# Kernel tuning notes

Measured on AMD Instinct MI355X. Metric: run time of the kernel, lower is better.

## Reference

```python
import math
import numpy as np
import jax, jax.numpy as jnp

LMAX1, LMAX2, LMAX3 = 20, 10, 5
B_IN, RES1, RES2, RES3 = 60, 20, 10, 6
BATCH = 8


def _fact(n):
    return math.factorial(n)


def wigner_d(l, betas):
    # small Wigner-d, complex-m ordering m=-l..l; betas: [N] -> [N, 2l+1, 2l+1]
    betas = np.asarray(betas, dtype=np.float64)
    cb, sb = np.cos(betas / 2.0), np.sin(betas / 2.0)
    d = np.zeros(betas.shape + (2 * l + 1, 2 * l + 1))
    for i, mp in enumerate(range(-l, l + 1)):
        for j, m in enumerate(range(-l, l + 1)):
            pref = math.sqrt(_fact(l + mp) * _fact(l - mp) * _fact(l + m) * _fact(l - m))
            val = np.zeros_like(betas)
            for k in range(max(0, m - mp), min(l + m, l - mp) + 1):
                den = _fact(l + m - k) * _fact(k) * _fact(mp - m + k) * _fact(l - mp - k)
                val = val + ((-1.0) ** (mp - m + k)) * (pref / den) * cb ** (2 * l + m - mp - 2 * k) * sb ** (mp - m + 2 * k)
            d[..., i, j] = val
    return d


def real_U(l):
    # complex SH -> real SH change of basis
    U = np.zeros((2 * l + 1, 2 * l + 1), dtype=np.complex128)
    U[l, l] = 1.0
    for m in range(1, l + 1):
        s = (-1.0) ** m
        U[l + m, l - m] = 1.0 / math.sqrt(2.0)
        U[l + m, l + m] = s / math.sqrt(2.0)
        U[l - m, l - m] = 1j / math.sqrt(2.0)
        U[l - m, l + m] = -1j * s / math.sqrt(2.0)
    return U


def wigner_d_real(l, betas):
    U = real_U(l)
    d = wigner_d(l, betas).astype(np.complex128)
    return np.einsum('ai,nij,bj->nab', U, d, U.conj()).real


def _trig(ang, l):
    m = np.arange(-l, l + 1)
    return np.cos(np.outer(ang, m)), np.sin(np.outer(ang, m))


def flat_wigner_points(lmax, a, b, g):
    # real Wigner D on arbitrary points via D = Z(alpha) d_real(beta) Z(gamma)
    blocks = []
    for l in range(lmax + 1):
        dr = wigner_d_real(l, b)  # [N,M,M]
        cA, sA = _trig(a, l)
        cG, sG = _trig(g, l)
        T = cG[:, None, :] * dr - sG[:, None, :] * dr[:, :, ::-1]
        D = cA[:, :, None] * T + sA[:, :, None] * T[:, ::-1, :]
        blocks.append(math.sqrt(2 * l + 1) * D.reshape(len(a), -1))
    return np.concatenate(blocks, -1).astype(np.float32)


def flat_wigner_grid(lmax, alphas, betas, gammas):
    # product-grid version, flatten order (alpha, beta, gamma)
    na, nb, ng = len(alphas), len(betas), len(gammas)
    blocks = []
    for l in range(lmax + 1):
        dr = wigner_d_real(l, betas)  # [nb,M,M]
        cA, sA = _trig(alphas, l)
        cG, sG = _trig(gammas, l)
        T = cG[None, :, None, :] * dr[:, None] - sG[None, :, None, :] * dr[:, None, :, ::-1]  # [nb,ng,M,M]
        D = cA[:, None, None, :, None] * T[None] + sA[:, None, None, :, None] * T[None, :, :, ::-1, :]
        blocks.append(math.sqrt(2 * l + 1) * D.reshape(na * nb * ng, -1))
    return np.concatenate(blocks, -1).astype(np.float32)


def sph_points(lmax, a, b):
    # component-normalized real SH: Y_l(alpha,beta) = sqrt(2l+1) D^l(alpha,beta,0)[:,m=0]
    cols = []
    for l in range(lmax + 1):
        dr = wigner_d_real(l, b)[:, :, l]
        cA, sA = _trig(a, l)
        cols.append(math.sqrt(2 * l + 1) * (cA * dr + sA * dr[:, ::-1]))
    return np.concatenate(cols, -1).astype(np.float32)


def sph_grid_cols(lmax, alphas, betas):
    cols = []
    for l in range(lmax + 1):
        dr = wigner_d_real(l, betas)[:, :, l]  # [nb,M]
        cA, sA = _trig(alphas, l)
        Y = cA[None] * dr[:, None] + sA[None] * dr[:, None, ::-1]  # [nb,na,M]
        cols.append(math.sqrt(2 * l + 1) * Y)
    return np.concatenate(cols, -1)


def so3_grid(n):
    a = np.arange(n) / n * 2 * math.pi
    b = (np.arange(n) + 0.5) / n * math.pi
    g = np.arange(n) / n * 2 * math.pi
    return a, b, g


def so3_transforms(lmax_in, lmax_out, n):
    a, b, g = so3_grid(n)
    D_in = flat_wigner_grid(lmax_in, a, b, g)
    D_out = flat_wigner_grid(lmax_out, a, b, g)
    qw = np.tile(np.sin(b)[None, :, None], (n, 1, n)).ravel() * math.pi / (2.0 * n ** 3)
    return jnp.asarray(D_in), jnp.asarray((qw[:, None] * D_out).astype(np.float32))


def s2_near_identity_grid(max_beta=math.pi / 8, n_alpha=8, n_beta=3):
    beta = np.arange(1, n_beta + 1) * max_beta / n_beta
    alpha = np.linspace(0, 2 * math.pi, n_alpha + 1)[:-1]
    A, B = np.meshgrid(alpha, beta, indexing='ij')
    return A.ravel(), B.ravel()


def so3_near_identity_grid(max_beta=math.pi / 8, max_gamma=2 * math.pi, n_alpha=8, n_beta=3, n_gamma=8):
    beta = np.arange(1, n_beta + 1) * max_beta / n_beta
    alpha = np.linspace(0, 2 * math.pi, n_alpha)[:-1]
    pre_gamma = np.linspace(-max_gamma, max_gamma, n_gamma)
    A, B, preC = np.meshgrid(alpha, beta, pre_gamma, indexing='ij')
    return A.ravel(), B.ravel(), (preC - A).ravel()


# ---- constant buffers (built once with numpy, like e3nn register_buffer) ----
_betas = (np.arange(B_IN) + 0.5) / B_IN * math.pi
_alphas = np.arange(B_IN) / B_IN * 2 * math.pi
_Y = sph_grid_cols(LMAX1, _alphas, _betas)  # [nb,na,441]
_qw = np.sin(_betas) * math.pi / (2.0 * B_IN * B_IN)
FROM_S2 = jnp.asarray((_Y * _qw[:, None, None]).reshape(B_IN * B_IN, -1).astype(np.float32))  # [3600,441]

_a2, _b2 = s2_near_identity_grid()
Y_K = jnp.asarray(sph_points(LMAX1, _a2, _b2))  # [24,441]
_a3, _b3, _g3 = so3_near_identity_grid()
D_K2 = jnp.asarray(flat_wigner_points(LMAX2, _a3, _b3, _g3))  # [168,1771]
D_K3 = jnp.asarray(flat_wigner_points(LMAX3, _a3, _b3, _g3))  # [168,286]

D1_IN, D1_BWD = so3_transforms(LMAX1, LMAX2, RES1)  # [8000,12341], [8000,1771]
D2_IN, D2_BWD = so3_transforms(LMAX2, LMAX3, RES2)  # [1000,1771],  [1000,286]
D3_IN, D3_BWD = so3_transforms(LMAX3, 0, RES3)      # [216,286],    [216,1]


def _s2_linear(x, psi, lmax):
    # x [B,f_in,(lmax+1)^2] (mult-1 per l) -> so3 irreps [B,f_out,sum(2l+1)^2]
    B, fi = x.shape[0], x.shape[1]
    outs = []
    for l in range(lmax + 1):
        s, e = l * l, (l + 1) * (l + 1)
        ol = jnp.einsum('bim,iou->boum', x[:, :, s:e], psi[:, :, s:e]) / math.sqrt(fi)
        outs.append(ol.reshape(B, ol.shape[1], -1))
    return jnp.concatenate(outs, axis=-1)


def _so3_linear(x, psi, lmax):
    # block per-l linear: mult (2l+1) -> mult (2l+1)
    B, fi = x.shape[0], x.shape[1]
    outs, off = [], 0
    for l in range(lmax + 1):
        d = 2 * l + 1
        xl = x[:, :, off:off + d * d].reshape(B, fi, d, d)
        pl = psi[:, :, off:off + d * d].reshape(fi, -1, d, d)
        ol = jnp.einsum('bium,iouv->bovm', xl, pl) / math.sqrt(fi * d)
        outs.append(ol.reshape(B, ol.shape[1], -1))
        off += d * d
    return jnp.concatenate(outs, axis=-1)


def _so3_act(x, D_in, D_bwd):
    # SO3Activation: to SO(3) grid, relu, back to (lower) band-limited coeffs
    f = jax.nn.relu(jnp.einsum('bfi,ni->bfn', x, D_in))
    return jnp.einsum('bfn,ni->bfi', f, D_bwd)


def _forward(x, conv1_w, conv2_w, conv3_w, fc_w1, fc_b1, fc_w2, fc_b2):
    B = x.shape[0]
    xg = jnp.swapaxes(x, -1, -2).reshape(B, -1)  # (beta, alpha) grid, flattened
    coeff = (xg @ FROM_S2)[:, None, :]           # FromS2Grid -> [B,1,441]
    psi1 = jnp.einsum('ni,xyn->xyi', Y_K, conv1_w) / math.sqrt(Y_K.shape[0])
    h = _s2_linear(coeff, psi1, LMAX1)           # [B,64,12341]
    h = _so3_act(h, D1_IN, D1_BWD)               # [B,64,1771]
    psi2 = jnp.einsum('ni,xyn->xyi', D_K2, conv2_w) / math.sqrt(D_K2.shape[0])
    h = _so3_linear(h, psi2, LMAX2)              # [B,128,1771]
    h = _so3_act(h, D2_IN, D2_BWD)               # [B,128,286]
    psi3 = jnp.einsum('ni,xyn->xyi', D_K3, conv3_w) / math.sqrt(D_K3.shape[0])
    h = _so3_linear(h, psi3, LMAX3)              # [B,256,286]
    h = _so3_act(h, D3_IN, D3_BWD)[:, :, 0]      # lmax_out=0 -> [B,256]
    h = jax.nn.relu(h @ fc_w1 + fc_b1)           # dropout is identity in eval
    return h @ fc_w2 + fc_b2


def setup_inputs() -> dict:
    key = jax.random.key(0)
    ks = jax.random.split(key, 6)
    return {
        'x': jax.random.normal(ks[0], (BATCH, B_IN, B_IN), dtype=jnp.float32),
        'conv1_w': jax.random.normal(ks[1], (1, 64, 24), dtype=jnp.float32),
        'conv2_w': jax.random.normal(ks[2], (64, 128, 168), dtype=jnp.float32),
        'conv3_w': jax.random.normal(ks[3], (128, 256, 168), dtype=jnp.float32),
        'fc_w1': jax.random.normal(ks[4], (256, 128), dtype=jnp.float32) / math.sqrt(256.0),
        'fc_b1': jnp.zeros((128,), jnp.float32),
        'fc_w2': jax.random.normal(ks[5], (128, 10), dtype=jnp.float32) / math.sqrt(128.0),
        'fc_b2': jnp.zeros((10,), jnp.float32),
    }


def reference(x, conv1_w, conv2_w, conv3_w, fc_w1, fc_b1, fc_w2, fc_b2):
    return _forward(x, conv1_w, conv2_w, conv3_w, fc_w1, fc_b1, fc_w2, fc_b2)
```

## Files before the change

kernel.cpp:

```cpp
#include <hip/hip_runtime.h>

#define PI_D 3.14159265358979323846

constexpr int S_L20 = 12341;
constexpr int S_L10 = 1771;
constexpr int S_L5  = 286;
constexpr int C_L20 = 441;

typedef float f4 __attribute__((ext_vector_type(4)));
typedef float f2 __attribute__((ext_vector_type(2)));
template<int W> struct VW;
template<> struct VW<4> { using T = f4; };
template<> struct VW<2> { using T = f2; };

__host__ __device__ __forceinline__ int loff(int l) { return l*(4*l*l-1)/3; }

__device__ __forceinline__ int isqrt_dev(int c) {
  int l = (int)sqrtf((float)c);
  while ((l+1)*(l+1) <= c) ++l;
  while (l*l > c) --l;
  return l;
}

__device__ double d_small(int l, int mp, int m, const double* cpw, const double* spw, const double* fact) {
// ... 11 lines not shown
__device__ double dr_elem(int l, int ap, int bp, const double* cpw, const double* spw, const double* fact) {
  const double IR2 = 0.70710678118654752440;
  if (ap == 0 && bp == 0) return d_small(l,0,0,cpw,spw,fact);
  if (bp == 0) {
    if (ap < 0) return 0.0;
    double sp = (ap&1)? -1.0: 1.0;
    return IR2*(d_small(l,-ap,0,cpw,spw,fact) + sp*d_small(l,ap,0,cpw,spw,fact));
  }
  if (ap == 0) {
    if (bp < 0) return 0.0;
    double sm = (bp&1)? -1.0: 1.0;
    return IR2*(d_small(l,0,-bp,cpw,spw,fact) + sm*d_small(l,0,bp,cpw,spw,fact));
  }
  if (ap > 0 && bp > 0) {
    double sp = (ap&1)?-1.0:1.0, sm = (bp&1)?-1.0:1.0;
    return 0.5*(d_small(l,-ap,-bp,cpw,spw,fact) + sm*d_small(l,-ap,bp,cpw,spw,fact)
              + sp*d_small(l,ap,-bp,cpw,spw,fact) + sp*sm*d_small(l,ap,bp,cpw,spw,fact));
  }
  if (ap < 0 && bp < 0) {
    int mp = -ap, m = -bp;
    double sp = (mp&1)?-1.0:1.0, sm = (m&1)?-1.0:1.0;
    return 0.5*(d_small(l,-mp,-m,cpw,spw,fact) - sm*d_small(l,-mp,m,cpw,spw,fact)
              - sp*d_small(l,mp,-m,cpw,spw,fact) + sp*sm*d_small(l,mp,m,cpw,spw,fact));
  }
  return 0.0;
}

__device__ double beta_of(int mode, int p, int gridn) {
  if (mode == 0) return (p + 0.5) * (PI_D / gridn);
  if (mode == 1) return (double)(((p >> 3) % 3) + 1) * (PI_D / 24.0);
  return (double)((p % 3) + 1) * (PI_D / 24.0);
}

__global__ __launch_bounds__(256) void k_drall(float* dr20g1, float* drK2, float* dr10g1, float* dr10g2,
                                               float* drK3, float* dr5g2, float* dr5g3, float* dr0g3) {
  __shared__ double cpw[44], spw[44], fact[44];
  int b = blockIdx.x;
  float* out; int lmax, S, mode, gridn, p, chunk;
  if (b < 260)      { out=dr20g1; lmax=20; S=S_L20; mode=0; gridn=20; p=b/13;        chunk=b%13; }
  else if (b < 596) { int i=b-260; out=drK2;   lmax=10; S=S_L10; mode=1; gridn=0;  p=i/2; chunk=i%2; }
  else if (b < 636) { int i=b-596; out=dr10g1; lmax=10; S=S_L10; mode=0; gridn=20; p=i/2; chunk=i%2; }
  else if (b < 656) { int i=b-636; out=dr10g2; lmax=10; S=S_L10; mode=0; gridn=10; p=i/2; chunk=i%2; }
  else if (b < 824) { int i=b-656; out=drK3;   lmax=5;  S=S_L5;  mode=1; gridn=0;  p=i;   chunk=0; }
  else if (b < 834) { int i=b-824; out=dr5g2;  lmax=5;  S=S_L5;  mode=0; gridn=10; p=i;   chunk=0; }
  else if (b < 840) { int i=b-834; out=dr5g3;  lmax=5;  S=S_L5;  mode=0; gridn=6;  p=i;   chunk=0; }
  else              { int i=b-840; out=dr0g3;  lmax=0;  S=1;     mode=0; gridn=6;  p=i;   chunk=0; }
  double beta_ = beta_of(mode, p, gridn);
  if (threadIdx.x == 0) {
    double cb_ = cos(beta_*0.5), sb_ = sin(beta_*0.5);
    cpw[0]=1.0; spw[0]=1.0; fact[0]=1.0;
    for (int i_=1;i_<44;++i_){cpw[i_]=cpw[i_-1]*cb_; spw[i_]=spw[i_-1]*sb_; fact[i_]=fact[i_-1]*(double)i_;}
  }
  __syncthreads();
  int base = chunk*1024;
  int end = min(S, base + 1024);
  for (int t = base + (int)threadIdx.x; t < end; t += 256) {
    int l = 0; while (l < lmax && t >= loff(l+1)) ++l;
    int j = t - loff(l), d = 2*l+1;
    int a = j/d, bb = j%d;
    double v = dr_elem(l, a-l, bb-l, cpw, spw, fact) * sqrt(2.0*l+1.0);
    out[(size_t)p*S + t] = (float)v;
  }
}

__global__ __launch_bounds__(256) void k_drc2(float* drc60, float* drc24) {
  __shared__ double cpw[44], spw[44], fact[44];
  int b = blockIdx.x;
  float* out; int mode, gridn, p;
  if (b < 60) { out = drc60; mode = 0; gridn = 60; p = b; }
  else        { out = drc24; mode = 2; gridn = 0;  p = b - 60; }
  double beta_ = beta_of(mode, p, gridn);
  if (threadIdx.x == 0) {
    double cb_ = cos(beta_*0.5), sb_ = sin(beta_*0.5);
    cpw[0]=1.0; spw[0]=1.0; fact[0]=1.0;
    for (int i_=1;i_<44;++i_){cpw[i_]=cpw[i_-1]*cb_; spw[i_]=spw[i_-1]*sb_; fact[i_]=fact[i_-1]*(double)i_;}
  }
  __syncthreads();
  for (int t = threadIdx.x; t < C_L20; t += 256) {
    int l = isqrt_dev(t);
    int u = t - l*l - l;
    double v;
    if (u < 0) v = 0.0;
    else if (u == 0) v = d_small(l,0,0,cpw,spw,fact);
    else {
      double sp = (u&1)? -1.0: 1.0;
      v = 0.70710678118654752440*(d_small(l,-u,0,cpw,spw,fact) + sp*d_small(l,u,0,cpw,spw,fact));
    }
    out[(size_t)p*C_L20 + t] = (float)(v * sqrt(2.0*l+1.0));
  }
}

__global__ __launch_bounds__(256) void k_trig3(float* __restrict__ t1c, float* __restrict__ t1s,
                                               float* __restrict__ t2c, float* __restrict__ t2s,
                                               float* __restrict__ t3c, float* __restrict__ t3s) {
  int t = blockIdx.x*256 + threadIdx.x;
  if (t < 420) {
    int k = t/20, ig = t%20;
    double ang = (double)k*(double)ig*(2.0*PI_D/20.0);
    t1c[t] = (float)cos(ang); t1s[t] = (float)sin(ang);
  } else if (t < 530) {
    int i = t-420, k = i/10, ig = i%10;
    double ang = (double)k*(double)ig*(2.0*PI_D/10.0);
    t2c[i] = (float)cos(ang); t2s[i] = (float)sin(ang);
  } else if (t < 566) {
    int i = t-530, k = i/6, ig = i%6;
    double ang = (double)k*(double)ig*(2.0*PI_D/6.0);
    t3c[i] = (float)cos(ang); t3s[i] = (float)sin(ang);
  }
}

__global__ __launch_bounds__(256) void k_slut2(unsigned* __restrict__ lut10, unsigned* __restrict__ lut5) {
  int t = blockIdx.x*256 + threadIdx.x;
  unsigned* lut; int s, lmax;
  if (t < S_L10) { lut = lut10; s = t; lmax = 10; }
  else if (t < S_L10 + S_L5) { lut = lut5; s = t - S_L10; lmax = 5; }
  else return;
  int l = 0; while (l < lmax && s >= loff(l+1)) ++l;
  int j = s - loff(l), d = 2*l+1;
  int u = j/d, v = j - u*d;
  lut[s] = (unsigned)l | ((unsigned)u<<8) | ((unsigned)v<<16);
}

__global__ __launch_bounds__(256) void k_fs2(const float* __restrict__ drc, float* __restrict__ FS2T) {
  int e = blockIdx.x*256 + threadIdx.x;
  if (e >= 441*3600) return;
  int c = e / 3600, k = e % 3600;
  int ia = k / 60, ib = k % 60;
  int l = isqrt_dev(c);
  int u = c - l*l - l;
  double alpha = (double)ia*(2.0*PI_D/60.0);
  double beta  = ((double)ib + 0.5)*(PI_D/60.0);
  double drp = (double)drc[ib*441 + c];
  double drn = (double)drc[ib*441 + (c - 2*u)];
  double val = cos((double)u*alpha)*drp + sin((double)u*alpha)*drn;
  FS2T[e] = (float)(val * (sin(beta)*PI_D/(2.0*60.0*60.0)));
}

__global__ __launch_bounds__(256) void k_coeff(const float* __restrict__ x, const float* __restrict__ fs2T,
                                               float* __restrict__ coeff) {
  int c = blockIdx.x;
  int tid = threadIdx.x;
  float acc[8] = {};
  const float* fr = fs2T + (size_t)c*3600;
  for (int k = tid; k < 3600; k += 256) {
    float w = fr[k];
#pragma unroll
    for (int b = 0; b < 8; ++b) acc[b] += w * x[b*3600 + k];
  }
  __shared__ float red[8][256];
#pragma unroll
  for (int b = 0; b < 8; ++b) red[b][tid] = acc[b];
  __syncthreads();
  for (int s = 128; s > 0; s >>= 1) {
    if (tid < s) {
#pragma unroll
      for (int b = 0; b < 8; ++b) red[b][tid] += red[b][tid+s];
    }
    __syncthreads();
  }
  if (tid < 8) coeff[tid*441 + c] = red[tid][0];
}

__global__ __launch_bounds__(256) void k_psi1(const float* __restrict__ drc24, const float* __restrict__ w1,
                                              float* __restrict__ psi1) {
  int e = blockIdx.x*256 + threadIdx.x;
  if (e >= 64*441) return;
  int o = e / 441, c = e % 441;
  int l = isqrt_dev(c);
  int u = c - l*l - l;
  float acc = 0.f;
  for (int p = 0; p < 24; ++p) {
    double alpha = (double)(p/3)*(PI_D/4.0);
    double y = cos((double)u*alpha)*(double)drc24[p*441+c] + sin((double)u*alpha)*(double)drc24[p*441 + (c-2*u)];
    acc += (float)y * w1[o*24 + p];
  }
  psi1[e] = acc * 0.20412414523193150818f;
}

__global__ __launch_bounds__(256) void k_dk2(const float* __restrict__ drk2, float* __restrict__ DK2,
                                             const float* __restrict__ drk3, float* __restrict__ DK3) {
  int e0 = blockIdx.x*256 + threadIdx.x;
  const float* drk; float* DK; int S, NP, lmax, e;
  if (e0 < 168*1772) { drk = drk2; DK = DK2; S = S_L10; NP = 1772; lmax = 10; e = e0; }
  else { e = e0 - 168*1772; if (e >= 168*288) return; drk = drk3; DK = DK3; S = S_L5; NP = 288; lmax = 5; }
  int n = e / NP, idx = e % NP;
  if (idx >= S) { DK[e] = 0.f; return; }
  int l = 0; while (l < lmax && idx >= loff(l+1)) ++l;
  int j = idx - loff(l), d = 2*l+1;
  int iu = j/d, im = j%d;
  int u = iu - l, m = im - l;
  int i3 = n/24, k3 = n%8;
  double alpha = (double)i3*(2.0*PI_D/7.0);
  double gamma = (-2.0*PI_D + (double)k3*(4.0*PI_D/7.0)) - alpha;
  const float* drb = drk + (size_t)n*S + loff(l);
  double d_um   = drb[iu*d+im];
  double d_umn  = drb[iu*d + (d-1-im)];
  double d_unm  = drb[(d-1-iu)*d + im];
  double d_unmn = drb[(d-1-iu)*d + (d-1-im)];
  double cA = cos((double)u*alpha), sA = sin((double)u*alpha);
  double cG = cos((double)m*gamma), sG = sin((double)m*gamma);
  DK[e] = (float)(cA*(cG*d_um - sG*d_umn) + sA*(cG*d_unm - sG*d_unmn));
}

__device__ __forceinline__ void gemm_body(const float* __restrict__ A, const float* __restrict__ B,
                                          const unsigned* __restrict__ lut, float* __restrict__ C,
                                          int M, int N, int NP, int K, int FO, int tm, int tn, float alpha,
                                          float (*As)[16][68], float (*Bs)[16][68], int tid) {
  int ty = tid/16, tx = tid%16;
  int arr = tid>>2, akq = (tid&3)*4;
  int bkk = tid>>4, bcq = (tid&15)*4;
  const float* Arow = A + (size_t)(tm + arr)*K;
  const f4 FZ = 0.f;
  float acc[4][4] = {};
  f4 ra, rb;
#define LOADC(k0)                                                        \
  if ((k0) + 16 <= K) {                                                  \
    ra = *(const f4*)&Arow[(k0) + akq];                                  \
    rb = *(const f4*)&B[(size_t)((k0) + bkk)*NP + tn + bcq];             \
  } else {                                                               \
    _Pragma("unroll")                                                    \
    for (int jj = 0; jj < 4; ++jj) {                                     \
      int k = (k0) + akq + jj;                                           \
      ra[jj] = (k < K) ? Arow[k] : 0.f;                                  \
    }                                                                    \
    int k2 = (k0) + bkk;                                                 \
    rb = (k2 < K) ? *(const f4*)&B[(size_t)k2*NP + tn + bcq] : FZ;       \
  }
#define STOREC(b)                                                        \
  {                                                                      \
    _Pragma("unroll")                                                    \
    for (int jj = 0; jj < 4; ++jj) As[b][akq+jj][arr] = ra[jj];          \
    *(f4*)&Bs[b][bkk][bcq] = rb;                                         \
  }
  LOADC(0);
  STOREC(0);
  __syncthreads();
  int cur = 0;
  for (int k0 = 0; k0 < K; k0 += 16) {
    bool nxt = (k0 + 16) < K;
    if (nxt) { LOADC(k0 + 16); }
#pragma unroll
    for (int kk = 0; kk < 16; ++kk) {
      f4 av = *(const f4*)&As[cur][kk][ty*4];
      f4 bv = *(const f4*)&Bs[cur][kk][tx*4];
#pragma unroll
      for (int q = 0; q < 4; ++q)
#pragma unroll
        for (int r2 = 0; r2 < 4; ++r2) acc[q][r2] += av[q]*bv[r2];
    }
    if (nxt) { STOREC(cur ^ 1); __syncthreads(); cur ^= 1; }
  }
#undef LOADC
#undef STOREC
  for (int q = 0; q < 4; ++q) {
    int r = tm + ty*4 + q; if (r >= M) continue;
    int i = r / FO, o = r - i*FO;
    for (int r2 = 0; r2 < 4; ++r2) {
      int c = tn + tx*4 + r2; if (c >= N) continue;
      unsigned e = lut[c];
      int l = e & 255, u = (e>>8)&255, v = (e>>16)&255;
      int d = 2*l+1;
      C[(size_t)M*loff(l) + (size_t)(i*d+u)*(FO*d) + o*d + v] = alpha*acc[q][r2];
    }
  }
}

__global__ __launch_bounds__(256) void k_gemm2(const float* __restrict__ A1, const float* __restrict__ B1,
                                               const unsigned* __restrict__ lut1, float* __restrict__ C1,
                                               int M1, int N1, int NP1, int FO1,
                                               const float* __restrict__ A2, const float* __restrict__ B2,
                                               const unsigned* __restrict__ lut2, float* __restrict__ C2,
                                               int M2, int N2, int NP2, int FO2,
                                               int K, int nbx1, int nb1, int nbx2, float alpha) {
  __shared__ __align__(16) float As[2][16][68], Bs[2][16][68];
  int bid = blockIdx.x, tid = threadIdx.x;
  if (bid < nb1) {
    int tm = (bid % nbx1)*64, tn = (bid / nbx1)*64;
    gemm_body(A1, B1, lut1, C1, M1, N1, NP1, K, FO1, tm, tn, alpha, As, Bs, tid);
  } else {
    bid -= nb1;
    int tm = (bid % nbx2)*64, tn = (bid / nbx2)*64;
    gemm_body(A2, B2, lut2, C2, M2, N2, NP2, K, FO2, tm, tn, alpha, As, Bs, tid);
  }
}

__global__ __launch_bounds__(256) void k_anapack(const float* __restrict__ part, const unsigned* __restrict__ lut,
                                                 float* __restrict__ hA, int FI, int S, int nch) {
  int e = blockIdx.x*256 + threadIdx.x;
  int total = 8*FI*S;
  if (e >= total) return;
  int bi = e / S, s = e - bi*S;
  float a = 0.f;
  for (int c = 0; c < nch; ++c) a += part[(size_t)c*total + e];
  unsigned u3 = lut[s];
  int l = u3 & 255, u = (u3>>8)&255, m = (u3>>16)&255;
  int d = 2*l+1;
  int b = bi / FI, i = bi - b*FI;
  hA[(size_t)8*FI*loff(l) + (size_t)(b*d+m)*(FI*d) + i*d + u] = a;
}

__global__ __launch_bounds__(256) void k_linsk(const float* __restrict__ hA, const float* __restrict__ psiP,
                                               float* __restrict__ part, int FI, int FO, int S,
                                               int maxNT, int KC) {
  int l = blockIdx.z;
  int d = 2*l+1, off = loff(l);
  int Ml = 8*d, Nl = FO*d, Kl = FI*d;
  int tm = blockIdx.x*64;
  int tn = ((int)blockIdx.y % maxNT)*64;
  int kci = (int)blockIdx.y / maxNT;
  int k0s = kci*KC;
  if (tm >= Ml || tn >= Nl || k0s >= Kl) return;
  int k1s = min(Kl, k0s + KC);
  float alpha = 1.0f/sqrtf((float)(FI*d));
  const float* Ab = hA + (size_t)8*FI*off;
  const float* Bb = psiP + (size_t)FI*FO*off;
// ... 19 lines not shown
  }
  LOADL(k0s);
  STOREL(0);
  __syncthreads();
  int cur = 0;
  for (int k0 = k0s; k0 < k1s; k0 += 16) {
    bool nxt = (k0 + 16) < k1s;
    if (nxt) { LOADL(k0 + 16); }
#pragma unroll
    for (int kk = 0; kk < 16; ++kk) {
      f4 av = *(const f4*)&As[cur][kk][ty*4];
      f4 bv = *(const f4*)&Bs[cur][kk][tx*4];
#pragma unroll
      for (int q = 0; q < 4; ++q)
#pragma unroll
        for (int r2 = 0; r2 < 4; ++r2) acc[q][r2] += av[q]*bv[r2];
    }
    if (nxt) { STOREL(cur ^ 1); __syncthreads(); cur ^= 1; }
  }
#undef LOADL
#undef STOREL
  size_t pbase = (size_t)kci * (size_t)8*FO*S;
  for (int q = 0; q < 4; ++q) {
    int r = tm + ty*4 + q; if (r >= Ml) continue;
    int b = r / d, m = r - b*d;
    for (int r2 = 0; r2 < 4; ++r2) {
      int c = tn + tx*4 + r2; if (c >= Nl) continue;
      int o = c / d, v = c - o*d;
      part[pbase + (size_t)(b*FO + o)*S + off + v*d + m] = alpha*acc[q][r2];
    }
  }
}

__global__ __launch_bounds__(256) void k_linred(const float* __restrict__ part, const unsigned* __restrict__ lut,
                                                float* __restrict__ hout, int FI, int FO, int S, int KC) {
  int e = blockIdx.x*256 + threadIdx.x;
  int total = 8*FO*S;
  if (e >= total) return;
  int s = e % S;
  int l = (int)(lut[s] & 255u);
  int Kl = FI*(2*l+1);
  int nch = (Kl + KC - 1)/KC;
  float a = 0.f;
  for (int c = 0; c < nch; ++c) a += part[(size_t)c*total + e];
  hout[e] = a;
}

template<int L, int NG, int F, int BS>
__global__ __launch_bounds__(BS) void k_syn1b(const float* __restrict__ psi1, const float* __restrict__ coeff,
                                              const float* __restrict__ drg,
                                              const float* __restrict__ gtck, const float* __restrict__ gtsk,
                                              float* __restrict__ fw) {
  constexpr int LH = L+1;
  constexpr int LH2 = LH*LH;
  constexpr int S = (L+1)*(2*L+1)*(2*L+3)/3;
  constexpr int IGB = 4;
  constexpr int NGB = NG / IGB;
  __shared__ float PF[4*LH2], Q1F[4*LH2], Q2F[4*LH2], Q3F[4*LH2];
  __shared__ __align__(16) float uni[4*C_L20];
  __shared__ __align__(16) float tck[LH*NG], tsk[LH*NG];
  float* psi_s  = uni;
  float* coef_s = uni + 2*C_L20;
  float* Rc = uni;
  float* Rs = uni + LH*NG;
  int ib = blockIdx.x, f0 = blockIdx.y*2, b0 = blockIdx.z*2;
  int tid = threadIdx.x;
  for (int t = tid; t < C_L20; t += BS) {
    psi_s[t]          = psi1[f0*C_L20 + t];
    psi_s[C_L20 + t]  = psi1[(f0+1)*C_L20 + t];
    coef_s[t]         = coeff[b0*C_L20 + t];
    coef_s[C_L20 + t] = coeff[(b0+1)*C_L20 + t];
  }
  for (int t = tid; t < LH*NG; t += BS) { tck[t] = gtck[t]; tsk[t] = gtsk[t]; }
  __syncthreads();
  const float* drb = drg + (size_t)ib*S;
  for (int t = tid; t < LH2; t += BS) {
    int i = t / LH, j = t % LH;
    int lmin = max(i, j);
    float P[4] = {}, Q1[4] = {}, Q2[4] = {}, Q3[4] = {};
    int d = 2*lmin+1;
// ... 56 lines not shown
      const float* Q2r = Q2F + cs*LH2 + i*LH;
      const float* Q3r = Q3F + cs*LH2 + i*LH;
      for (int k = 0; k <= L; ++k) {
        float p = Pr[k], q1 = Q1r[k], q2 = Q2r[k], q3 = Q3r[k];
        f4 c = *(const f4*)(tck + k*NG + ig0);
        f4 s = *(const f4*)(tsk + k*NG + ig0);
        rc += c*p + s*q1;
        rs += c*q2 + s*q3;
      }
      *(f4*)(Rc + i*NG + ig0) = rc;
      *(f4*)(Rs + i*NG + ig0) = rs;
    }
    __syncthreads();
    size_t obase = (((size_t)(b0+cb)*F + (f0+cf))*NG + ib)*(size_t)(NG*NG);
    for (int t = tid; t < NG*NGB; t += BS) {
      int ia = t / NGB, ig0 = (t % NGB)*IGB;
      f4 acc = 0.f;
      for (int k = 0; k <= L; ++k) {
        float ca = tck[k*NG + ia], sa = tsk[k*NG + ia];
        f4 rc = *(const f4*)(Rc + k*NG + ig0);
        f4 rs = *(const f4*)(Rs + k*NG + ig0);
        acc += ca*rc - sa*rs;
      }
      f4 res;
#pragma unroll
      for (int jj = 0; jj < 4; ++jj) res[jj] = fmaxf(acc[jj], 0.0f) * qwv;
      *(f4*)(fw + obase + ia*NG + ig0) = res;
    }
    __syncthreads();
  }
}

template<int L, int NG, int F, int BS>
__global__ __launch_bounds__(BS) void k_syn(const float* __restrict__ hin,
                                            const float* __restrict__ drg,
                                            const float* __restrict__ gtck, const float* __restrict__ gtsk,
                                            float* __restrict__ fw) {
  constexpr int LH = L+1;
  constexpr int LH2 = LH*LH;
  constexpr int S = (L+1)*(2*L+1)*(2*L+3)/3;
  constexpr int RCSZ = LH*NG;
  constexpr int UNI = (S > 2*RCSZ) ? S : 2*RCSZ;
  constexpr int IGB = (NG % 4 == 0) ? 4 : 2;
  constexpr int NGB = NG / IGB;
  using VecT = typename VW<IGB>::T;
  __shared__ float PF[LH2], Q1F[LH2], Q2F[LH2], Q3F[LH2];
  __shared__ __align__(16) float uni[UNI];
  __shared__ __align__(16) float tck[LH*NG], tsk[LH*NG];
  float* hrow = uni;
  float* Rc = uni;
  float* Rs = uni + RCSZ;
  int ib = blockIdx.x, f = blockIdx.y, b = blockIdx.z;
  int tid = threadIdx.x;
  for (int t = tid; t < S; t += BS) hrow[t] = hin[((size_t)b*F + f)*S + t];
  for (int t = tid; t < LH*NG; t += BS) { tck[t] = gtck[t]; tsk[t] = gtsk[t]; }
  __syncthreads();
  const float* drb = drg + (size_t)ib*S;
  for (int t = tid; t < LH2; t += BS) {
    int i = t / LH, j = t % LH;
    int lmin = max(i, j);
    float P = 0.f, Q1 = 0.f, Q2 = 0.f, Q3 = 0.f;
    int d = 2*lmin+1;
    int j2 = 2*j;
    int drip = loff(lmin) + (lmin+i)*d + (lmin-j);
    int drim = loff(lmin) + (lmin-i)*d + (lmin-j);
    for (int l = lmin; l <= L; ++l) {
      float ap_ = drb[drip], app = drb[drip + j2];
      float am_ = 0.f, amp = 0.f;
      if (i > 0) { am_ = drb[drim]; amp = drb[drim + j2]; }
      float hp1 = hrow[drip], hp2 = hrow[drip + j2];
      float hm1 = hrow[drim], hm2 = hrow[drim + j2];
      P  += ap_*hp1 + app*hp2 + am_*hm1 + amp*hm2;
      Q1 += app*hp1 - ap_*hp2 + amp*hm1 - am_*hm2;
      Q2 += ap_*hm1 + app*hm2 - am_*hp1 - amp*hp2;
      Q3 += app*hm1 - ap_*hm2 - amp*hp1 + am_*hp2;
      drip += d*d + d + 2*(l+i) + 3;
      drim += d*d + d + 2*(l-i) + 3;
      d += 2;
    }
    if (j == 0) { P *= 0.5f; Q2 *= 0.5f; }
    PF[t] = P; Q1F[t] = Q1; Q2F[t] = Q2; Q3F[t] = Q3;
  }
  __syncthreads();
  for (int t = tid; t < LH*NGB; t += BS) {
    int i = t / NGB, ig0 = (t % NGB)*IGB;
    VecT rc = 0.f, rs = 0.f;
    const float* Pr  = PF  + i*LH;
// ... 180 lines not shown

  float* base = (float*)d_ws;
  size_t off = 0;
  auto alloc = [&](size_t n) -> float* { float* p = base + off; off += (n + 63) & ~(size_t)63; return p; };

  float* drc60  = alloc((size_t)60*441);
  float* drc24  = alloc((size_t)24*441);
  float* fs2T   = alloc((size_t)441*3600);
  float* psi1   = alloc((size_t)64*441);
  float* coeff  = alloc((size_t)8*441);
  float* drK2   = alloc((size_t)168*S_L10);
  float* drK3   = alloc((size_t)168*S_L5);
  float* dk2    = alloc((size_t)168*1772 + 64);
  float* dk3    = alloc((size_t)168*288 + 64);
  float* psi2P  = alloc((size_t)8192*S_L10);
  float* psi3P  = alloc((size_t)32768*S_L5);
  float* dr20g1 = alloc((size_t)20*S_L20);
  float* dr10g1 = alloc((size_t)20*S_L10);
  float* dr10g2 = alloc((size_t)10*S_L10);
  float* dr5g2  = alloc((size_t)10*S_L5);
  float* dr5g3  = alloc((size_t)6*S_L5);
  float* dr0g3  = alloc(6);
  float* t1ck   = alloc((size_t)21*20);
  float* t1sk   = alloc((size_t)21*20);
  float* t2ck   = alloc((size_t)11*10);
  float* t2sk   = alloc((size_t)11*10);
  float* t3ck   = alloc((size_t)6*6);
  float* t3sk   = alloc((size_t)6*6);
  float* lut10  = alloc((size_t)S_L10);
  float* lut5   = alloc((size_t)S_L5);
  float* fwbuf  = alloc((size_t)8*64*8000);
  float* scr    = alloc((size_t)3*8*128*S_L10);
  float* hA2    = alloc((size_t)8*64*S_L10);
  float* h2b    = alloc((size_t)8*128*S_L10);
  float* hA3    = alloc((size_t)8*128*S_L5);
  float* h3b    = alloc((size_t)8*256*S_L5);
  float* h4     = alloc((size_t)8*256);
  if (off * sizeof(float) > ws_size) return;

  const float inv_s168 = 0.07715167498104595f;
  const int KC = 512;

  k_drc2 <<<dim3(84),  256, 0, stream>>>(drc60, drc24);
  k_drall<<<dim3(846), 256, 0, stream>>>(dr20g1, drK2, dr10g1, dr10g2, drK3, dr5g2, dr5g3, dr0g3);
  k_trig3<<<dim3(3),   256, 0, stream>>>(t1ck, t1sk, t2ck, t2sk, t3ck, t3sk);
  k_slut2<<<dim3((S_L10+S_L5+255)/256), 256, 0, stream>>>((unsigned*)lut10, (unsigned*)lut5);
  k_fs2  <<<dim3((441*3600+255)/256), 256, 0, stream>>>(drc60, fs2T);
  k_psi1 <<<dim3((64*441+255)/256),   256, 0, stream>>>(drc24, w1, psi1);
  k_dk2  <<<dim3((168*1772+168*288+255)/256), 256, 0, stream>>>(drK2, dk2, drK3, dk3);

  k_coeff<<<dim3(441), 256, 0, stream>>>(x, fs2T, coeff);
  k_gemm2<<<dim3(3584 + 2560), 256, 0, stream>>>(
      w2, dk2, (const unsigned*)lut10, psi2P, 8192,  S_L10, 1772, 128,
      w3, dk3, (const unsigned*)lut5,  psi3P, 32768, S_L5,  288,  256,
      168, 128, 3584, 512, inv_s168);

  k_syn1b<20,20,64,256><<<dim3(20,32,4), 256, 0, stream>>>(psi1, coeff, dr20g1, t1ck, t1sk, fwbuf);
  k_ana<10,20,64,4,256><<<dim3(64,8,5),  256, 0, stream>>>(fwbuf, dr10g1, t1ck, t1sk, scr);
  k_anapack<<<dim3((8*64*S_L10+255)/256), 256, 0, stream>>>(scr, (const unsigned*)lut10, hA2, 64, S_L10, 5);
  k_linsk<<<dim3(3, 42*3, 11), 256, 0, stream>>>(hA2, psi2P, scr, 64, 128, S_L10, 42, KC);
  k_linred<<<dim3((8*128*S_L10+255)/256), 256, 0, stream>>>(scr, (const unsigned*)lut10, h2b, 64, 128, S_L10, KC);
  k_syn<10,10,128,128><<<dim3(10,128,8), 128, 0, stream>>>(h2b, dr10g2, t2ck, t2sk, fwbuf);
  k_ana<5,10,128,5,128><<<dim3(128,8,2),  128, 0, stream>>>(fwbuf, dr5g2, t2ck, t2sk, scr);
  k_anapack<<<dim3((8*128*S_L5+255)/256), 256, 0, stream>>>(scr, (const unsigned*)lut5, hA3, 128, S_L5, 2);
  k_linsk<<<dim3(2, 44*3, 6), 256, 0, stream>>>(hA3, psi3P, scr, 128, 256, S_L5, 44, KC);
  k_linred<<<dim3((8*256*S_L5+255)/256), 256, 0, stream>>>(scr, (const unsigned*)lut5, h3b, 128, 256, S_L5, KC);
  k_syn<5,6,256,64><<<dim3(6,256,8), 64, 0, stream>>>(h3b, dr5g3, t3ck, t3sk, fwbuf);
  k_ana<0,6,256,6,64><<<dim3(256,8,1), 64, 0, stream>>>(fwbuf, dr0g3, t3ck, t3sk, h4);
  k_fc<<<dim3(1), 1024, 0, stream>>>(h4, fcw1, fcb1, fcw2, fcb2, out);
}
```

Measured before the change: 671.7 us.

## Merge table-setup kernels, fold coeff into GEMM launch, fuse split-K reduce into synthesis

Combines the four independent table-building kernels into one launch and the three dependent table kernels (fs2, psi1, dk) into a second launch. The coefficient reduction now runs as extra blocks of the combined GEMM kernel, reusing its shared memory. The separate split-K reduction kernels are removed, and the synthesis kernels sum the partial chunks while loading each row, using hardcoded thresholds. This cuts the number of launches and one intermediate write/read round trip. The cost is more branching per block and thresholds that must match the chunking rule.

```diff
diff --git a/kernel.cpp b/kernel.cpp
--- a/kernel.cpp
+++ b/kernel.cpp
@@ -67,174 +67,148 @@
   return (double)((p % 3) + 1) * (PI_D / 24.0);
 }
 
-__global__ __launch_bounds__(256) void k_drall(float* dr20g1, float* drK2, float* dr10g1, float* dr10g2,
-                                               float* drK3, float* dr5g2, float* dr5g3, float* dr0g3) {
+__global__ __launch_bounds__(256) void k_tables(float* dr20g1, float* drK2, float* dr10g1, float* dr10g2,
+                                                float* drK3, float* dr5g2, float* dr5g3, float* dr0g3,
+                                                float* drc60, float* drc24,
+                                                float* t1c, float* t1s, float* t2c, float* t2s,
+                                                float* t3c, float* t3s,
+                                                unsigned* lut10, unsigned* lut5) {
   __shared__ double cpw[44], spw[44], fact[44];
   int b = blockIdx.x;
-  float* out; int lmax, S, mode, gridn, p, chunk;
-  if (b < 260)      { out=dr20g1; lmax=20; S=S_L20; mode=0; gridn=20; p=b/13;        chunk=b%13; }
-  else if (b < 596) { int i=b-260; out=drK2;   lmax=10; S=S_L10; mode=1; gridn=0;  p=i/2; chunk=i%2; }
-  else if (b < 636) { int i=b-596; out=dr10g1; lmax=10; S=S_L10; mode=0; gridn=20; p=i/2; chunk=i%2; }
-  else if (b < 656) { int i=b-636; out=dr10g2; lmax=10; S=S_L10; mode=0; gridn=10; p=i/2; chunk=i%2; }
-  else if (b < 824) { int i=b-656; out=drK3;   lmax=5;  S=S_L5;  mode=1; gridn=0;  p=i;   chunk=0; }
-  else if (b < 834) { int i=b-824; out=dr5g2;  lmax=5;  S=S_L5;  mode=0; gridn=10; p=i;   chunk=0; }
-  else if (b < 840) { int i=b-834; out=dr5g3;  lmax=5;  S=S_L5;  mode=0; gridn=6;  p=i;   chunk=0; }
-  else              { int i=b-840; out=dr0g3;  lmax=0;  S=1;     mode=0; gridn=6;  p=i;   chunk=0; }
-  double beta_ = beta_of(mode, p, gridn);
-  if (threadIdx.x == 0) {
-    double cb_ = cos(beta_*0.5), sb_ = sin(beta_*0.5);
-    cpw[0]=1.0; spw[0]=1.0; fact[0]=1.0;
-    for (int i_=1;i_<44;++i_){cpw[i_]=cpw[i_-1]*cb_; spw[i_]=spw[i_-1]*sb_; fact[i_]=fact[i_-1]*(double)i_;}
-  }
-  __syncthreads();
-  int base = chunk*1024;
-  int end = min(S, base + 1024);
-  for (int t = base + (int)threadIdx.x; t < end; t += 256) {
-    int l = 0; while (l < lmax && t >= loff(l+1)) ++l;
-    int j = t - loff(l), d = 2*l+1;
-    int a = j/d, bb = j%d;
-    double v = dr_elem(l, a-l, bb-l, cpw, spw, fact) * sqrt(2.0*l+1.0);
-    out[(size_t)p*S + t] = (float)v;
-  }
-}
-
-__global__ __launch_bounds__(256) void k_drc2(float* drc60, float* drc24) {
-  __shared__ double cpw[44], spw[44], fact[44];
-  int b = blockIdx.x;
-  float* out; int mode, gridn, p;
-  if (b < 60) { out = drc60; mode = 0; gridn = 60; p = b; }
-  else        { out = drc24; mode = 2; gridn = 0;  p = b - 60; }
-  double beta_ = beta_of(mode, p, gridn);
-  if (threadIdx.x == 0) {
-    double cb_ = cos(beta_*0.5), sb_ = sin(beta_*0.5);
-    cpw[0]=1.0; spw[0]=1.0; fact[0]=1.0;
-    for (int i_=1;i_<44;++i_){cpw[i_]=cpw[i_-1]*cb_; spw[i_]=spw[i_-1]*sb_; fact[i_]=fact[i_-1]*(double)i_;}
-  }
-  __syncthreads();
-  for (int t = threadIdx.x; t < C_L20; t += 256) {
-    int l = isqrt_dev(t);
-    int u = t - l*l - l;
-    double v;
-    if (u < 0) v = 0.0;
-    else if (u == 0) v = d_small(l,0,0,cpw,spw,fact);
-    else {
-      double sp = (u&1)? -1.0: 1.0;
-      v = 0.70710678118654752440*(d_small(l,-u,0,cpw,spw,fact) + sp*d_small(l,u,0,cpw,spw,fact));
-    }
-    out[(size_t)p*C_L20 + t] = (float)(v * sqrt(2.0*l+1.0));
-  }
-}
-
-__global__ __launch_bounds__(256) void k_trig3(float* __restrict__ t1c, float* __restrict__ t1s,
-                                               float* __restrict__ t2c, float* __restrict__ t2s,
-                                               float* __restrict__ t3c, float* __restrict__ t3s) {
-  int t = blockIdx.x*256 + threadIdx.x;
-  if (t < 420) {
-    int k = t/20, ig = t%20;
-    double ang = (double)k*(double)ig*(2.0*PI_D/20.0);
-    t1c[t] = (float)cos(ang); t1s[t] = (float)sin(ang);
-  } else if (t < 530) {
-    int i = t-420, k = i/10, ig = i%10;
-    double ang = (double)k*(double)ig*(2.0*PI_D/10.0);
-    t2c[i] = (float)cos(ang); t2s[i] = (float)sin(ang);
-  } else if (t < 566) {
-    int i = t-530, k = i/6, ig = i%6;
-    double ang = (double)k*(double)ig*(2.0*PI_D/6.0);
-    t3c[i] = (float)cos(ang); t3s[i] = (float)sin(ang);
-  }
-}
-
-__global__ __launch_bounds__(256) void k_slut2(unsigned* __restrict__ lut10, unsigned* __restrict__ lut5) {
-  int t = blockIdx.x*256 + threadIdx.x;
-  unsigned* lut; int s, lmax;
-  if (t < S_L10) { lut = lut10; s = t; lmax = 10; }
-  else if (t < S_L10 + S_L5) { lut = lut5; s = t - S_L10; lmax = 5; }
-  else return;
-  int l = 0; while (l < lmax && s >= loff(l+1)) ++l;
-  int j = s - loff(l), d = 2*l+1;
-  int u = j/d, v = j - u*d;
-  lut[s] = (unsigned)l | ((unsigned)u<<8) | ((unsigned)v<<16);
-}
-
-__global__ __launch_bounds__(256) void k_fs2(const float* __restrict__ drc, float* __restrict__ FS2T) {
-  int e = blockIdx.x*256 + threadIdx.x;
-  if (e >= 441*3600) return;
-  int c = e / 3600, k = e % 3600;
-  int ia = k / 60, ib = k % 60;
-  int l = isqrt_dev(c);
-  int u = c - l*l - l;
-  double alpha = (double)ia*(2.0*PI_D/60.0);
-  double beta  = ((double)ib + 0.5)*(PI_D/60.0);
-  double drp = (double)drc[ib*441 + c];
-  double drn = (double)drc[ib*441 + (c - 2*u)];
-  double val = cos((double)u*alpha)*drp + sin((double)u*alpha)*drn;
-  FS2T[e] = (float)(val * (sin(beta)*PI_D/(2.0*60.0*60.0)));
-}
-
-__global__ __launch_bounds__(256) void k_coeff(const float* __restrict__ x, const float* __restrict__ fs2T,
-                                               float* __restrict__ coeff) {
-  int c = blockIdx.x;
   int tid = threadIdx.x;
-  float acc[8] = {};
-  const float* fr = fs2T + (size_t)c*3600;
-  for (int k = tid; k < 3600; k += 256) {
-    float w = fr[k];
-#pragma unroll
-    for (int b = 0; b < 8; ++b) acc[b] += w * x[b*3600 + k];
-  }
-  __shared__ float red[8][256];
-#pragma unroll
-  for (int b = 0; b < 8; ++b) red[b][tid] = acc[b];
-  __syncthreads();
-  for (int s = 128; s > 0; s >>= 1) {
-    if (tid < s) {
-#pragma unroll
-      for (int b = 0; b < 8; ++b) red[b][tid] += red[b][tid+s];
-    }
-    __syncthreads();
-  }
-  if (tid < 8) coeff[tid*441 + c] = red[tid][0];
-}
-
-__global__ __launch_bounds__(256) void k_psi1(const float* __restrict__ drc24, const float* __restrict__ w1,
-                                              float* __restrict__ psi1) {
-  int e = blockIdx.x*256 + threadIdx.x;
-  if (e >= 64*441) return;
-  int o = e / 441, c = e % 441;
-  int l = isqrt_dev(c);
-  int u = c - l*l - l;
-  float acc = 0.f;
-  for (int p = 0; p < 24; ++p) {
-    double alpha = (double)(p/3)*(PI_D/4.0);
-    double y = cos((double)u*alpha)*(double)drc24[p*441+c] + sin((double)u*alpha)*(double)drc24[p*441 + (c-2*u)];
-    acc += (float)y * w1[o*24 + p];
-  }
-  psi1[e] = acc * 0.20412414523193150818f;
-}
-
-__global__ __launch_bounds__(256) void k_dk2(const float* __restrict__ drk2, float* __restrict__ DK2,
-                                             const float* __restrict__ drk3, float* __restrict__ DK3) {
-  int e0 = blockIdx.x*256 + threadIdx.x;
-  const float* drk; float* DK; int S, NP, lmax, e;
-  if (e0 < 168*1772) { drk = drk2; DK = DK2; S = S_L10; NP = 1772; lmax = 10; e = e0; }
-  else { e = e0 - 168*1772; if (e >= 168*288) return; drk = drk3; DK = DK3; S = S_L5; NP = 288; lmax = 5; }
-  int n = e / NP, idx = e % NP;
-  if (idx >= S) { DK[e] = 0.f; return; }
-  int l = 0; while (l < lmax && idx >= loff(l+1)) ++l;
-  int j = idx - loff(l), d = 2*l+1;
-  int iu = j/d, im = j%d;
-  int u = iu - l, m = im - l;
-  int i3 = n/24, k3 = n%8;
-  double alpha = (double)i3*(2.0*PI_D/7.0);
-  double gamma = (-2.0*PI_D + (double)k3*(4.0*PI_D/7.0)) - alpha;
-  const float* drb = drk + (size_t)n*S + loff(l);
-  double d_um   = drb[iu*d+im];
-  double d_umn  = drb[iu*d + (d-1-im)];
-  double d_unm  = drb[(d-1-iu)*d + im];
-  double d_unmn = drb[(d-1-iu)*d + (d-1-im)];
-  double cA = cos((double)u*alpha), sA = sin((double)u*alpha);
-  double cG = cos((double)m*gamma), sG = sin((double)m*gamma);
-  DK[e] = (float)(cA*(cG*d_um - sG*d_umn) + sA*(cG*d_unm - sG*d_unmn));
+  if (b < 846) {
+    float* out; int lmax, S, mode, gridn, p, chunk;
+    if (b < 260)      { out=dr20g1; lmax=20; S=S_L20; mode=0; gridn=20; p=b/13;        chunk=b%13; }
+    else if (b < 596) { int i=b-260; out=drK2;   lmax=10; S=S_L10; mode=1; gridn=0;  p=i/2; chunk=i%2; }
+    else if (b < 636) { int i=b-596; out=dr10g1; lmax=10; S=S_L10; mode=0; gridn=20; p=i/2; chunk=i%2; }
+    else if (b < 656) { int i=b-636; out=dr10g2; lmax=10; S=S_L10; mode=0; gridn=10; p=i/2; chunk=i%2; }
+    else if (b < 824) { int i=b-656; out=drK3;   lmax=5;  S=S_L5;  mode=1; gridn=0;  p=i;   chunk=0; }
+    else if (b < 834) { int i=b-824; out=dr5g2;  lmax=5;  S=S_L5;  mode=0; gridn=10; p=i;   chunk=0; }
+    else if (b < 840) { int i=b-834; out=dr5g3;  lmax=5;  S=S_L5;  mode=0; gridn=6;  p=i;   chunk=0; }
+    else              { int i=b-840; out=dr0g3;  lmax=0;  S=1;     mode=0; gridn=6;  p=i;   chunk=0; }
+    double beta_ = beta_of(mode, p, gridn);
+    if (tid == 0) {
+      double cb_ = cos(beta_*0.5), sb_ = sin(beta_*0.5);
+      cpw[0]=1.0; spw[0]=1.0; fact[0]=1.0;
+      for (int i_=1;i_<44;++i_){cpw[i_]=cpw[i_-1]*cb_; spw[i_]=spw[i_-1]*sb_; fact[i_]=fact[i_-1]*(double)i_;}
+    }
+    __syncthreads();
+    int base = chunk*1024;
+    int end = min(S, base + 1024);
+    for (int t = base + tid; t < end; t += 256) {
+      int l = 0; while (l < lmax && t >= loff(l+1)) ++l;
+      int j = t - loff(l), d = 2*l+1;
+      int a = j/d, bb = j%d;
+      double v = dr_elem(l, a-l, bb-l, cpw, spw, fact) * sqrt(2.0*l+1.0);
+      out[(size_t)p*S + t] = (float)v;
+    }
+  } else if (b < 930) {
+    int bb = b - 846;
+    float* out; int mode, gridn, p;
+    if (bb < 60) { out = drc60; mode = 0; gridn = 60; p = bb; }
+    else         { out = drc24; mode = 2; gridn = 0;  p = bb - 60; }
+    double beta_ = beta_of(mode, p, gridn);
+    if (tid == 0) {
+      double cb_ = cos(beta_*0.5), sb_ = sin(beta_*0.5);
+      cpw[0]=1.0; spw[0]=1.0; fact[0]=1.0;
+      for (int i_=1;i_<44;++i_){cpw[i_]=cpw[i_-1]*cb_; spw[i_]=spw[i_-1]*sb_; fact[i_]=fact[i_-1]*(double)i_;}
+    }
+    __syncthreads();
+    for (int t = tid; t < C_L20; t += 256) {
+      int l = isqrt_dev(t);
+      int u = t - l*l - l;
+      double v;
+      if (u < 0) v = 0.0;
+      else if (u == 0) v = d_small(l,0,0,cpw,spw,fact);
+      else {
+        double sp = (u&1)? -1.0: 1.0;
+        v = 0.70710678118654752440*(d_small(l,-u,0,cpw,spw,fact) + sp*d_small(l,u,0,cpw,spw,fact));
+      }
+      out[(size_t)p*C_L20 + t] = (float)(v * sqrt(2.0*l+1.0));
+    }
+  } else if (b < 933) {
+    int t = (b - 930)*256 + tid;
+    if (t < 420) {
+      int k = t/20, ig = t%20;
+      double ang = (double)k*(double)ig*(2.0*PI_D/20.0);
+      t1c[t] = (float)cos(ang); t1s[t] = (float)sin(ang);
+    } else if (t < 530) {
+      int i = t-420, k = i/10, ig = i%10;
+      double ang = (double)k*(double)ig*(2.0*PI_D/10.0);
+      t2c[i] = (float)cos(ang); t2s[i] = (float)sin(ang);
+    } else if (t < 566) {
+      int i = t-530, k = i/6, ig = i%6;
+      double ang = (double)k*(double)ig*(2.0*PI_D/6.0);
+      t3c[i] = (float)cos(ang); t3s[i] = (float)sin(ang);
+    }
+  } else {
+    int t = (b - 933)*256 + tid;
+    unsigned* lut; int s, lmax;
+    if (t < S_L10) { lut = lut10; s = t; lmax = 10; }
+    else if (t < S_L10 + S_L5) { lut = lut5; s = t - S_L10; lmax = 5; }
+    else return;
+    int l = 0; while (l < lmax && s >= loff(l+1)) ++l;
+    int j = s - loff(l), d = 2*l+1;
+    int u = j/d, v = j - u*d;
+    lut[s] = (unsigned)l | ((unsigned)u<<8) | ((unsigned)v<<16);
+  }
+}
+
+__global__ __launch_bounds__(256) void k_tab2(const float* __restrict__ drc60, float* __restrict__ FS2T,
+                                              const float* __restrict__ drc24, const float* __restrict__ w1,
+                                              float* __restrict__ psi1,
+                                              const float* __restrict__ drk2, float* __restrict__ DK2,
+                                              const float* __restrict__ drk3, float* __restrict__ DK3) {
+  int b = blockIdx.x, tid = threadIdx.x;
+  if (b < 6202) {
+    int e = b*256 + tid;
+    if (e >= 441*3600) return;
+    int c = e / 3600, k = e % 3600;
+    int ia = k / 60, ib = k % 60;
+    int l = isqrt_dev(c);
+    int u = c - l*l - l;
+    double alpha = (double)ia*(2.0*PI_D/60.0);
+    double beta  = ((double)ib + 0.5)*(PI_D/60.0);
+    double drp = (double)drc60[ib*441 + c];
+    double drn = (double)drc60[ib*441 + (c - 2*u)];
+    double val = cos((double)u*alpha)*drp + sin((double)u*alpha)*drn;
+    FS2T[e] = (float)(val * (sin(beta)*PI_D/(2.0*60.0*60.0)));
+  } else if (b < 6313) {
+    int e = (b - 6202)*256 + tid;
+    if (e >= 64*441) return;
+    int o = e / 441, c = e % 441;
+    int l = isqrt_dev(c);
+    int u = c - l*l - l;
+    float acc = 0.f;
+    for (int p = 0; p < 24; ++p) {
+      double alpha = (double)(p/3)*(PI_D/4.0);
+      double y = cos((double)u*alpha)*(double)drc24[p*441+c] + sin((double)u*alpha)*(double)drc24[p*441 + (c-2*u)];
+      acc += (float)y * w1[o*24 + p];
+    }
+    psi1[e] = acc * 0.20412414523193150818f;
+  } else {
+    int e0 = (b - 6313)*256 + tid;
+    const float* drk; float* DK; int S, NP, lmax, e;
+    if (e0 < 168*1772) { drk = drk2; DK = DK2; S = S_L10; NP = 1772; lmax = 10; e = e0; }
+    else { e = e0 - 168*1772; if (e >= 168*288) return; drk = drk3; DK = DK3; S = S_L5; NP = 288; lmax = 5; }
+    int n = e / NP, idx = e % NP;
+    if (idx >= S) { DK[e] = 0.f; return; }
+    int l = 0; while (l < lmax && idx >= loff(l+1)) ++l;
+    int j = idx - loff(l), d = 2*l+1;
+    int iu = j/d, im = j%d;
+    int u = iu - l, m = im - l;
+    int i3 = n/24, k3 = n%8;
+    double alpha = (double)i3*(2.0*PI_D/7.0);
+    double gamma = (-2.0*PI_D + (double)k3*(4.0*PI_D/7.0)) - alpha;
+    const float* drb = drk + (size_t)n*S + loff(l);
+    double d_um   = drb[iu*d+im];
+    double d_umn  = drb[iu*d + (d-1-im)];
+    double d_unm  = drb[(d-1-iu)*d + im];
+    double d_unmn = drb[(d-1-iu)*d + (d-1-im)];
+    double cA = cos((double)u*alpha), sA = sin((double)u*alpha);
+    double cG = cos((double)m*gamma), sG = sin((double)m*gamma);
+    DK[e] = (float)(cA*(cG*d_um - sG*d_umn) + sA*(cG*d_unm - sG*d_unmn));
+  }
 }
 
 __device__ __forceinline__ void gemm_body(const float* __restrict__ A, const float* __restrict__ B,
@@ -300,22 +274,45 @@
   }
 }
 
-__global__ __launch_bounds__(256) void k_gemm2(const float* __restrict__ A1, const float* __restrict__ B1,
+__global__ __launch_bounds__(256) void k_gemmc(const float* __restrict__ A1, const float* __restrict__ B1,
                                                const unsigned* __restrict__ lut1, float* __restrict__ C1,
                                                int M1, int N1, int NP1, int FO1,
                                                const float* __restrict__ A2, const float* __restrict__ B2,
                                                const unsigned* __restrict__ lut2, float* __restrict__ C2,
                                                int M2, int N2, int NP2, int FO2,
-                                               int K, int nbx1, int nb1, int nbx2, float alpha) {
+                                               int K, int nbx1, int nb1, int nbx2, int nb12, float alpha,
+                                               const float* __restrict__ x, const float* __restrict__ fs2T,
+                                               float* __restrict__ coeff) {
   __shared__ __align__(16) float As[2][16][68], Bs[2][16][68];
   int bid = blockIdx.x, tid = threadIdx.x;
   if (bid < nb1) {
     int tm = (bid % nbx1)*64, tn = (bid / nbx1)*64;
     gemm_body(A1, B1, lut1, C1, M1, N1, NP1, K, FO1, tm, tn, alpha, As, Bs, tid);
-  } else {
+  } else if (bid < nb12) {
     bid -= nb1;
     int tm = (bid % nbx2)*64, tn = (bid / nbx2)*64;
     gemm_body(A2, B2, lut2, C2, M2, N2, NP2, K, FO2, tm, tn, alpha, As, Bs, tid);
+  } else {
+    int c = bid - nb12;
+    float acc[8] = {};
+    const float* fr = fs2T + (size_t)c*3600;
+    for (int k = tid; k < 3600; k += 256) {
+      float w = fr[k];
+#pragma unroll
+      for (int b = 0; b < 8; ++b) acc[b] += w * x[b*3600 + k];
+    }
+    float* red = (float*)As;
+#pragma unroll
+    for (int b = 0; b < 8; ++b) red[b*256 + tid] = acc[b];
+    __syncthreads();
+    for (int s = 128; s > 0; s >>= 1) {
+      if (tid < s) {
+#pragma unroll
+        for (int b = 0; b < 8; ++b) red[b*256 + tid] += red[b*256 + tid + s];
+      }
+      __syncthreads();
+    }
+    if (tid < 8) coeff[tid*441 + c] = red[tid*256];
   }
 }
 
@@ -401,20 +398,6 @@
   }
 }
 
-__global__ __launch_bounds__(256) void k_linred(const float* __restrict__ part, const unsigned* __restrict__ lut,
-                                                float* __restrict__ hout, int FI, int FO, int S, int KC) {
-  int e = blockIdx.x*256 + threadIdx.x;
-  int total = 8*FO*S;
-  if (e >= total) return;
-  int s = e % S;
-  int l = (int)(lut[s] & 255u);
-  int Kl = FI*(2*l+1);
-  int nch = (Kl + KC - 1)/KC;
-  float a = 0.f;
-  for (int c = 0; c < nch; ++c) a += part[(size_t)c*total + e];
-  hout[e] = a;
-}
-
 template<int L, int NG, int F, int BS>
 __global__ __launch_bounds__(BS) void k_syn1b(const float* __restrict__ psi1, const float* __restrict__ coeff,
                                               const float* __restrict__ drg,
@@ -537,7 +520,7 @@
 }
 
 template<int L, int NG, int F, int BS>
-__global__ __launch_bounds__(BS) void k_syn(const float* __restrict__ hin,
+__global__ __launch_bounds__(BS) void k_syn(const float* __restrict__ part, int thr1, int thr2, int total,
                                             const float* __restrict__ drg,
                                             const float* __restrict__ gtck, const float* __restrict__ gtsk,
                                             float* __restrict__ fw) {
@@ -557,7 +540,13 @@
   float* Rs = uni + RCSZ;
   int ib = blockIdx.x, f = blockIdx.y, b = blockIdx.z;
   int tid = threadIdx.x;
-  for (int t = tid; t < S; t += BS) hrow[t] = hin[((size_t)b*F + f)*S + t];
+  for (int t = tid; t < S; t += BS) {
+    size_t e = ((size_t)b*F + f)*S + t;
+    float a = part[e];
+    if (t >= thr1) a += part[(size_t)total + e];
+    if (t >= thr2) a += part[2*(size_t)total + e];
+    hrow[t] = a;
+  }
   for (int t = tid; t < LH*NG; t += BS) { tck[t] = gtck[t]; tsk[t] = gtsk[t]; }
   __syncthreads();
   const float* drb = drg + (size_t)ib*S;
@@ -804,40 +793,31 @@
   float* fwbuf  = alloc((size_t)8*64*8000);
   float* scr    = alloc((size_t)3*8*128*S_L10);
   float* hA2    = alloc((size_t)8*64*S_L10);
-  float* h2b    = alloc((size_t)8*128*S_L10);
   float* hA3    = alloc((size_t)8*128*S_L5);
-  float* h3b    = alloc((size_t)8*256*S_L5);
   float* h4     = alloc((size_t)8*256);
   if (off * sizeof(float) > ws_size) return;
 
   const float inv_s168 = 0.07715167498104595f;
   const int KC = 512;
 
-  k_drc2 <<<dim3(84),  256, 0, stream>>>(drc60, drc24);
-  k_drall<<<dim3(846), 256, 0, stream>>>(dr20g1, drK2, dr10g1, dr10g2, drK3, dr5g2, dr5g3, dr0g3);
-  k_trig3<<<dim3(3),   256, 0, stream>>>(t1ck, t1sk, t2ck, t2sk, t3ck, t3sk);
-  k_slut2<<<dim3((S_L10+S_L5+255)/256), 256, 0, stream>>>((unsigned*)lut10, (unsigned*)lut5);
-  k_fs2  <<<dim3((441*3600+255)/256), 256, 0, stream>>>(drc60, fs2T);
-  k_psi1 <<<dim3((64*441+255)/256),   256, 0, stream>>>(drc24, w1, psi1);
-  k_dk2  <<<dim3((168*1772+168*288+255)/256), 256, 0, stream>>>(drK2, dk2, drK3, dk3);
-
-  k_coeff<<<dim3(441), 256, 0, stream>>>(x, fs2T, coeff);
-  k_gemm2<<<dim3(3584 + 2560), 256, 0, stream>>>(
+  k_tables<<<dim3(942), 256, 0, stream>>>(dr20g1, drK2, dr10g1, dr10g2, drK3, dr5g2, dr5g3, dr0g3,
+                                          drc60, drc24, t1ck, t1sk, t2ck, t2sk, t3ck, t3sk,
+                                          (unsigned*)lut10, (unsigned*)lut5);
+  k_tab2<<<dim3(7665), 256, 0, stream>>>(drc60, fs2T, drc24, w1, psi1, drK2, dk2, drK3, dk3);
+  k_gemmc<<<dim3(3584 + 2560 + 441), 256, 0, stream>>>(
       w2, dk2, (const unsigned*)lut10, psi2P, 8192,  S_L10, 1772, 128,
       w3, dk3, (const unsigned*)lut5,  psi3P, 32768, S_L5,  288,  256,
-      168, 128, 3584, 512, inv_s168);
+      168, 128, 3584, 512, 6144, inv_s168, x, fs2T, coeff);
 
   k_syn1b<20,20,64,256><<<dim3(20,32,4), 256, 0, stream>>>(psi1, coeff, dr20g1, t1ck, t1sk, fwbuf);
   k_ana<10,20,64,4,256><<<dim3(64,8,5),  256, 0, stream>>>(fwbuf, dr10g1, t1ck, t1sk, scr);
   k_anapack<<<dim3((8*64*S_L10+255)/256), 256, 0, stream>>>(scr, (const unsigned*)lut10, hA2, 64, S_L10, 5);
   k_linsk<<<dim3(3, 42*3, 11), 256, 0, stream>>>(hA2, psi2P, scr, 64, 128, S_L10, 42, KC);
-  k_linred<<<dim3((8*128*S_L10+255)/256), 256, 0, stream>>>(scr, (const unsigned*)lut10, h2b, 64, 128, S_L10, KC);
-  k_syn<10,10,128,128><<<dim3(10,128,8), 128, 0, stream>>>(h2b, dr10g2, t2ck, t2sk, fwbuf);
+  k_syn<10,10,128,128><<<dim3(10,128,8), 128, 0, stream>>>(scr, 84, 680, 8*128*S_L10, dr10g2, t2ck, t2sk, fwbuf);
   k_ana<5,10,128,5,128><<<dim3(128,8,2),  128, 0, stream>>>(fwbuf, dr5g2, t2ck, t2sk, scr);
   k_anapack<<<dim3((8*128*S_L5+255)/256), 256, 0, stream>>>(scr, (const unsigned*)lut5, hA3, 128, S_L5, 2);
   k_linsk<<<dim3(2, 44*3, 6), 256, 0, stream>>>(hA3, psi3P, scr, 128, 256, S_L5, 44, KC);
-  k_linred<<<dim3((8*256*S_L5+255)/256), 256, 0, stream>>>(scr, (const unsigned*)lut5, h3b, 128, 256, S_L5, KC);
-  k_syn<5,6,256,64><<<dim3(6,256,8), 64, 0, stream>>>(h3b, dr5g3, t3ck, t3sk, fwbuf);
+  k_syn<5,6,256,64><<<dim3(6,256,8), 64, 0, stream>>>(scr, 10, 84, 8*256*S_L5, dr5g3, t3ck, t3sk, fwbuf);
   k_ana<0,6,256,6,64><<<dim3(256,8,1), 64, 0, stream>>>(fwbuf, dr0g3, t3ck, t3sk, h4);
   k_fc<<<dim3(1), 1024, 0, stream>>>(h4, fcw1, fcb1, fcw2, fcb2, out);
 }
```

New measurement: 635.2 us. -5.4%, faster.
